# Performance work log

Measured on AMD Instinct MI355X. Metric: run time of the kernel, lower is better.

Reference implementation:

```python
import jax, jax.numpy as jnp
import numpy as np

B, S, DM = 2, 2048, 1024
H, DH = 16, 64
SCALE = jnp.sqrt(jnp.float32(DH))  # dot_scale = sqrt(dim_head)


def setup_inputs() -> dict:
    key = jax.random.key(0)
    ks = jax.random.split(key, 9)
    std = 1.0 / np.sqrt(DM)
    x = jax.random.normal(ks[0], (B, S, DM), dtype=jnp.float32)
    Wq = jax.random.uniform(ks[1], (DM, DM), jnp.float32, -std, std)
    bq = jax.random.uniform(ks[2], (DM,), jnp.float32, -std, std)
    Wk = jax.random.uniform(ks[3], (DM, DM), jnp.float32, -std, std)
    bk = jax.random.uniform(ks[4], (DM,), jnp.float32, -std, std)
    Wv = jax.random.uniform(ks[5], (DM, DM), jnp.float32, -std, std)
    bv = jax.random.uniform(ks[6], (DM,), jnp.float32, -std, std)
    Wo = jax.random.uniform(ks[7], (DM, DM), jnp.float32, -std, std)
    bo = jax.random.uniform(ks[8], (DM,), jnp.float32, -std, std)
    # causal mask: 1 = masked (future positions), broadcast over batch
    causal = jnp.triu(jnp.ones((S, S), dtype=jnp.int32), k=1)
    attention_mask = jnp.broadcast_to(causal, (B, S, S))
    return {"x": x, "Wq": Wq, "bq": bq, "Wk": Wk, "bk": bk,
            "Wv": Wv, "bv": bv, "Wo": Wo, "bo": bo,
            "attention_mask": attention_mask}


def reference(x, Wq, bq, Wk, bk, Wv, bv, Wo, bo, attention_mask):
    # Linear layers (torch nn.Linear: y = x @ W^T + b)
    q = (x @ Wq.T + bq).reshape(B, S, H, DH).transpose(0, 2, 1, 3)  # (B,H,S,DH)
    k = (x @ Wk.T + bk).reshape(B, S, H, DH).transpose(0, 2, 1, 3)  # (B,H,S,DH)
    v = (x @ Wv.T + bv).reshape(B, S, H, DH).transpose(0, 2, 1, 3)  # (B,H,S,DH)
    # scores: (B,H,S,S), then mask==1 -> -inf, softmax over last dim
    scores = jnp.einsum('bhsd,bhtd->bhst', q, k) / SCALE
    mask = attention_mask[:, None, :, :]  # (B,1,S,S)
    scores = jnp.where(mask == 1, -jnp.inf, scores)
    attn = jax.nn.softmax(scores, axis=-1)
    # dropout is identity in eval mode
    ctx = jnp.einsum('bhst,bhtd->bshd', attn, v).reshape(B, S, H * DH)
    return ctx @ Wo.T + bo
```

## Files before the change

kernel.cpp:

```cpp
#include <hip/hip_runtime.h>
#include <stdint.h>

typedef unsigned short u16;
typedef __attribute__((ext_vector_type(8))) short bf16x8;
typedef __attribute__((ext_vector_type(4))) float f32x4;

#define BATCH 2
#define S_LEN 2048
#define DMODEL 1024
#define NH 16
#define DHEAD 64
#define MTOT 4096
#define QSCALE 0.18033688011112042f

#define GL2LDS(g, l) \
  __builtin_amdgcn_global_load_lds((const __attribute__((address_space(1))) void*)(g), \
                                   (__attribute__((address_space(3))) void*)(l), 16, 0, 0)

__device__ __forceinline__ u16 f2bf(float x) {
  union { float f; uint32_t u; } v; v.f = x;
  uint32_t r = v.u + 0x7fffu + ((v.u >> 16) & 1u);
  return (u16)(r >> 16);
}
__device__ __forceinline__ u16 f2bf_fast(float x) {
  union { float f; uint32_t u; } v; v.f = x;
  return (u16)((v.u + 0x8000u) >> 16);
}

struct CvtArgs {
  const float* src[5];
  u16* dst[5];
};

__global__ __launch_bounds__(256) void cvt_all(CvtArgs a) {
  int bx = blockIdx.x;
  int region, off;
  if (bx < 4096) { region = 0; off = bx; }
  else { region = 1 + ((bx - 4096) >> 10); off = (bx - 4096) & 1023; }
  const float* s = a.src[region];
  u16* d = a.dst[region];
  int i = (off * 256 + threadIdx.x) * 4;
  float4 v = *(const float4*)(s + i);
  uint2 pk;
  pk.x = (uint32_t)f2bf(v.x) | ((uint32_t)f2bf(v.y) << 16);
  pk.y = (uint32_t)f2bf(v.z) | ((uint32_t)f2bf(v.w) << 16);
  *(uint2*)(d + i) = pk;
}

__device__ __forceinline__ void gemm_body(const u16* __restrict__ A,
                                          const u16* __restrict__ W,
                                          const float* __restrict__ bias,
                                          void* __restrict__ out,
                                          int mode, float scale) {
  __shared__ u16 As[128 * 32];
  __shared__ u16 Bs[128 * 32];
  const int tid = threadIdx.x;
  const int m0 = blockIdx.y * 128;
  const int n0 = blockIdx.x * 128;
  const int wave = tid >> 6, lane = tid & 63;
  const int wm = (wave >> 1) * 64, wn = (wave & 1) * 64;
  const int quad = lane >> 4, l15 = lane & 15;

  const int row0 = tid >> 2, g0 = ((tid & 3) ^ (row0 & 3)) * 8;
  const int row1 = (tid + 256) >> 2, g1 = ((tid & 3) ^ (row1 & 3)) * 8;
  const int lb0 = wave * 512;
  const int lb1 = 2048 + wave * 512;
  const int xk = (quad ^ (l15 & 3)) * 8;

  f32x4 acc[4][4] = {};

  for (int kt = 0; kt < DMODEL; kt += 32) {
    GL2LDS(A + (size_t)(m0 + row0) * DMODEL + kt + g0, As + lb0);
    GL2LDS(A + (size_t)(m0 + row1) * DMODEL + kt + g1, As + lb1);
    GL2LDS(W + (size_t)(n0 + row0) * DMODEL + kt + g0, Bs + lb0);
    GL2LDS(W + (size_t)(n0 + row1) * DMODEL + kt + g1, Bs + lb1);
    __syncthreads();
    bf16x8 af[4], bfr[4];
#pragma unroll
    for (int bi = 0; bi < 4; ++bi)
      af[bi] = *(const bf16x8*)(&As[(wm + bi * 16 + l15) * 32 + xk]);
#pragma unroll
    for (int bj = 0; bj < 4; ++bj)
      bfr[bj] = *(const bf16x8*)(&Bs[(wn + bj * 16 + l15) * 32 + xk]);
#pragma unroll
    for (int bi = 0; bi < 4; ++bi)
#pragma unroll
      for (int bj = 0; bj < 4; ++bj)
        acc[bi][bj] = __builtin_amdgcn_mfma_f32_16x16x32_bf16(af[bi], bfr[bj], acc[bi][bj], 0, 0, 0);
    __syncthreads();
  }

#pragma unroll
  for (int bi = 0; bi < 4; ++bi) {
#pragma unroll
    for (int bj = 0; bj < 4; ++bj) {
      int n = n0 + wn + bj * 16 + l15;
      float bval = bias[n];
#pragma unroll
      for (int r = 0; r < 4; ++r) {
        int m = m0 + wm + bi * 16 + quad * 4 + r;
        float v = (acc[bi][bj][r] + bval) * scale;
        u16 bvu = f2bf(v);
        int b = m >> 11, s = m & 2047;
        int h = n >> 6, d = n & 63;
        size_t bh = (size_t)(b * NH + h);
        if (mode == 1)
          ((u16*)out)[(bh * S_LEN + s) * DHEAD + d] = bvu;
        else
          ((u16*)out)[((bh * 256 + (s >> 3)) * 64 + d) * 8 + (s & 7)] = bvu;
      }
    }
  }
}

struct QKVArgs {
  const u16* w[3];
  const float* b[3];
  u16* o[3];
};

__global__ __launch_bounds__(256) void qkv_gemm(const u16* __restrict__ xb, QKVArgs a) {
  int z = blockIdx.z;
  int mode = (z == 2) ? 2 : 1;
  float scale = (z == 0) ? QSCALE : 1.0f;
  gemm_body(xb, a.w[z], a.b[z], a.o[z], mode, scale);
}

__global__ __launch_bounds__(256) void out_gemm(const u16* __restrict__ A,
                                                const u16* __restrict__ W,
                                                const float* __restrict__ bias,
                                                float* __restrict__ out) {
  __shared__ u16 As[128 * 32];
  __shared__ u16 Bs[64 * 32];
  const int tid = threadIdx.x;
  const int m0 = blockIdx.y * 128;
  const int n0 = blockIdx.x * 64;
  const int wave = tid >> 6, lane = tid & 63;
  const int wm = (wave >> 1) * 64, wn = (wave & 1) * 32;
  const int quad = lane >> 4, l15 = lane & 15;

  const int row0 = tid >> 2, g0 = ((tid & 3) ^ (row0 & 3)) * 8;
  const int row1 = (tid + 256) >> 2, g1 = ((tid & 3) ^ (row1 & 3)) * 8;
  const int lb0 = wave * 512;
  const int lb1 = 2048 + wave * 512;
  const int xk = (quad ^ (l15 & 3)) * 8;

  f32x4 acc[4][2] = {};

  for (int kt = 0; kt < DMODEL; kt += 32) {
    GL2LDS(A + (size_t)(m0 + row0) * DMODEL + kt + g0, As + lb0);
    GL2LDS(A + (size_t)(m0 + row1) * DMODEL + kt + g1, As + lb1);
    GL2LDS(W + (size_t)(n0 + row0) * DMODEL + kt + g0, Bs + lb0);
    __syncthreads();
    bf16x8 af[4], bfr[2];
#pragma unroll
    for (int bi = 0; bi < 4; ++bi)
      af[bi] = *(const bf16x8*)(&As[(wm + bi * 16 + l15) * 32 + xk]);
#pragma unroll
    for (int bj = 0; bj < 2; ++bj)
      bfr[bj] = *(const bf16x8*)(&Bs[(wn + bj * 16 + l15) * 32 + xk]);
#pragma unroll
    for (int bi = 0; bi < 4; ++bi)
#pragma unroll
      for (int bj = 0; bj < 2; ++bj)
        acc[bi][bj] = __builtin_amdgcn_mfma_f32_16x16x32_bf16(af[bi], bfr[bj], acc[bi][bj], 0, 0, 0);
    __syncthreads();
  }

#pragma unroll
  for (int bi = 0; bi < 4; ++bi) {
#pragma unroll
    for (int bj = 0; bj < 2; ++bj) {
      int n = n0 + wn + bj * 16 + l15;
      float bval = bias[n];
#pragma unroll
      for (int r = 0; r < 4; ++r) {
        int m = m0 + wm + bi * 16 + quad * 4 + r;
        out[(size_t)m * DMODEL + n] = acc[bi][bj][r] + bval;
      }
    }
  }
}

__global__ __launch_bounds__(256) void attn(const u16* __restrict__ Q,
                                            const u16* __restrict__ Kg,
                                            const u16* __restrict__ Vt8,
                                            u16* __restrict__ ctx) {
  __shared__ u16 Kd[2][128 * 64];
  __shared__ u16 Vd[2][64 * 128];
  __shared__ u16 Ps[64 * 80];
  const int tid = threadIdx.x;
  const int qp = blockIdx.x >> 5;
  const int bh = blockIdx.x & 31;
  const int wave = tid >> 6, lane = tid & 63;
  const int quad = lane >> 4, l15 = lane & 15;
  const size_t base = (size_t)bh * S_LEN * DHEAD;
  const int b = bh >> 4, h = bh & 15;
  const int xk7 = l15 & 7;

#define STAGE(kt_, pb)                                                                   \
  do {                                                                                   \
    _Pragma("unroll")                                                                    \
    for (int i_ = 0; i_ < 4; ++i_) {                                                     \
      int c_ = tid + 256 * i_;                                                           \
      int row_ = c_ >> 3, g_ = ((c_ & 7) ^ (row_ & 7)) * 8;                              \
      GL2LDS(Kg + base + (size_t)((kt_) * 128 + row_) * 64 + g_,                         \
             &Kd[pb][0] + i_ * 2048 + wave * 512);                                       \
      GL2LDS(Vt8 + base + (size_t)((kt_) * 1024 + c_) * 8,                               \
             &Vd[pb][0] + i_ * 2048 + wave * 512);                                       \
    }                                                                                    \
  } while (0)

  for (int half = 0; half < 2; ++half) {
    const int qt = half ? (31 - qp) : qp;
    const int qrow = qt * 64 + wave * 16 + l15;
    bf16x8 qf0 = *(const bf16x8*)(Q + base + (size_t)qrow * DHEAD + quad * 8);
    bf16x8 qf1 = *(const bf16x8*)(Q + base + (size_t)qrow * DHEAD + 32 + quad * 8);

    float l_part[4] = {0.f, 0.f, 0.f, 0.f};
    f32x4 o[4] = {};

    const int ktmax = qt >> 1;
    STAGE(0, 0);

    for (int kt = 0; kt <= ktmax; ++kt) {
      const int p = kt & 1;
      __syncthreads();
      if (kt < ktmax) STAGE(kt + 1, p ^ 1);

      const bool diag = (kt == ktmax);
      const int qg_max = qt * 64 + wave * 16 + 15;
      f32x4 s_acc[8];
#pragma unroll
      for (int bj = 0; bj < 8; ++bj) {
        if (diag && (kt * 128 + bj * 16 > qg_max)) {
          s_acc[bj] = f32x4{-1e30f, -1e30f, -1e30f, -1e30f};
          continue;
        }
        const int krow = (bj * 16 + l15) * 64;
        bf16x8 kf0 = *(const bf16x8*)(&Kd[p][krow + ((quad ^ xk7) * 8)]);
        bf16x8 kf1 = *(const bf16x8*)(&Kd[p][krow + (((quad + 4) ^ xk7) * 8)]);
        f32x4 t = {0.f, 0.f, 0.f, 0.f};
        t = __builtin_amdgcn_mfma_f32_16x16x32_bf16(qf0, kf0, t, 0, 0, 0);
        t = __builtin_amdgcn_mfma_f32_16x16x32_bf16(qf1, kf1, t, 0, 0, 0);
        s_acc[bj] = t;
      }

      if (diag) {
#pragma unroll
        for (int bj = 0; bj < 8; ++bj) {
          int kg = kt * 128 + bj * 16 + l15;
#pragma unroll
          for (int r = 0; r < 4; ++r) {
            int qg = qt * 64 + wave * 16 + quad * 4 + r;
            if (kg > qg) s_acc[bj][r] = -1e30f;
          }
        }
      }

#pragma unroll
      for (int ph = 0; ph < 2; ++ph) {
        if (diag && (kt * 128 + ph * 64 > qg_max)) continue;
#pragma unroll
        for (int bj2 = 0; bj2 < 4; ++bj2) {
          int bj = ph * 4 + bj2;
#pragma unroll
          for (int r = 0; r < 4; ++r) {
            float pv = exp2f(s_acc[bj][r]);
            l_part[r] += pv;
            Ps[(wave * 16 + quad * 4 + r) * 80 + bj2 * 16 + l15] = f2bf_fast(pv);
          }
        }
#pragma unroll
        for (int kk2 = 0; kk2 < 2; ++kk2) {
          bf16x8 pf = *(const bf16x8*)(&Ps[(wave * 16 + l15) * 80 + kk2 * 32 + quad * 8]);
          int kk = ph * 2 + kk2;
#pragma unroll
          for (int dj = 0; dj < 4; ++dj) {
            bf16x8 vf = *(const bf16x8*)(&Vd[p][((kk * 4 + quad) * 64 + dj * 16 + l15) * 8]);
            o[dj] = __builtin_amdgcn_mfma_f32_16x16x32_bf16(pf, vf, o[dj], 0, 0, 0);
          }
        }
      }
    }

    __syncthreads();

#pragma unroll
    for (int r = 0; r < 4; ++r) {
      float s = l_part[r];
      s += __shfl_xor(s, 1, 64);
      s += __shfl_xor(s, 2, 64);
      s += __shfl_xor(s, 4, 64);
      s += __shfl_xor(s, 8, 64);
      float inv = 1.0f / s;
      int srow = qt * 64 + wave * 16 + quad * 4 + r;
      size_t rowbase = ((size_t)b * S_LEN + srow) * DMODEL + h * DHEAD;
#pragma unroll
      for (int dj = 0; dj < 4; ++dj)
        ctx[rowbase + dj * 16 + l15] = f2bf(o[dj][r] * inv);
    }
  }
#undef STAGE
}

extern "C" void kernel_launch(void* const* d_in, const int* in_sizes, int n_in,
                              void* d_out, int out_size, void* d_ws, size_t ws_size,
                              hipStream_t stream) {
  const float* x  = (const float*)d_in[0];
  const float* Wq = (const float*)d_in[1];
  const float* bq = (const float*)d_in[2];
  const float* Wk = (const float*)d_in[3];
  const float* bk = (const float*)d_in[4];
  const float* Wv = (const float*)d_in[5];
  const float* bv = (const float*)d_in[6];
  const float* Wo = (const float*)d_in[7];
  const float* bo = (const float*)d_in[8];
  float* out = (float*)d_out;

  char* ws = (char*)d_ws;
  const size_t MB = 1u << 20;
  u16* xb   = (u16*)(ws + 0);
  u16* ctxb = xb;
  u16* wqb  = (u16*)(ws + 8 * MB);
  u16* wkb  = (u16*)(ws + 10 * MB);
  u16* wvb  = (u16*)(ws + 12 * MB);
  u16* wob  = (u16*)(ws + 14 * MB);
  u16* qb   = (u16*)(ws + 16 * MB);
  u16* kb   = (u16*)(ws + 24 * MB);
  u16* vtb  = (u16*)(ws + 32 * MB);

  CvtArgs c;
  c.src[0] = x;  c.dst[0] = xb;
  c.src[1] = Wq; c.dst[1] = wqb;
  c.src[2] = Wk; c.dst[2] = wkb;
  c.src[3] = Wv; c.dst[3] = wvb;
  c.src[4] = Wo; c.dst[4] = wob;
  cvt_all<<<4096 + 4 * 1024, 256, 0, stream>>>(c);

  QKVArgs a;
  a.w[0] = wqb; a.w[1] = wkb; a.w[2] = wvb;
  a.b[0] = bq;  a.b[1] = bk;  a.b[2] = bv;
  a.o[0] = qb;  a.o[1] = kb;  a.o[2] = vtb;
  qkv_gemm<<<dim3(DMODEL / 128, MTOT / 128, 3), 256, 0, stream>>>(xb, a);

  attn<<<512, 256, 0, stream>>>(qb, kb, vtb, ctxb);

  out_gemm<<<dim3(DMODEL / 64, MTOT / 128), 256, 0, stream>>>(ctxb, wob, bo, out);
}
```

Baseline: 208.6 us.

## Shrink attention KV tile to 64 and launch one block per query tile

The attention kernel now uses 64-row K/V tiles instead of 128 and launches 1024 blocks, each owning a single query tile, instead of 512 blocks that each processed a pair of tiles. Query tiles are assigned to blocks with a zig-zag ordering to balance causal work across the grid, and the P scratch buffer gets an XOR swizzle in place of padding. Shared memory per block drops, and launch_bounds now requests 4 blocks per CU, which should raise occupancy and trim wasted work on the diagonal tile. In exchange there are more loop iterations and barriers per unit of work, and register pressure is capped by the occupancy hint.

After: 210.0 us. No clear change (+0.7%).

```diff
diff --git a/kernel.cpp b/kernel.cpp
--- a/kernel.cpp
+++ b/kernel.cpp
@@ -182,16 +182,19 @@
   }
 }
 
-__global__ __launch_bounds__(256) void attn(const u16* __restrict__ Q,
-                                            const u16* __restrict__ Kg,
-                                            const u16* __restrict__ Vt8,
-                                            u16* __restrict__ ctx) {
-  __shared__ u16 Kd[2][128 * 64];
-  __shared__ u16 Vd[2][64 * 128];
-  __shared__ u16 Ps[64 * 80];
+__global__ __launch_bounds__(256, 4) void attn(const u16* __restrict__ Q,
+                                               const u16* __restrict__ Kg,
+                                               const u16* __restrict__ Vt8,
+                                               u16* __restrict__ ctx) {
+  __shared__ u16 Kd[2][64 * 64];
+  __shared__ u16 Vd[2][64 * 64];
+  __shared__ u16 Ps[64 * 64];
   const int tid = threadIdx.x;
-  const int qp = blockIdx.x >> 5;
+  const int g = blockIdx.x >> 5;
   const int bh = blockIdx.x & 31;
+  const int gv = g & 7;
+  int qt = (g & 8) ? (15 - gv) : gv;
+  if (g & 16) qt += 16;
   const int wave = tid >> 6, lane = tid & 63;
   const int quad = lane >> 4, l15 = lane & 15;
   const size_t base = (size_t)bh * S_LEN * DHEAD;
@@ -201,105 +204,98 @@
 #define STAGE(kt_, pb)                                                                   \
   do {                                                                                   \
     _Pragma("unroll")                                                                    \
-    for (int i_ = 0; i_ < 4; ++i_) {                                                     \
+    for (int i_ = 0; i_ < 2; ++i_) {                                                     \
       int c_ = tid + 256 * i_;                                                           \
       int row_ = c_ >> 3, g_ = ((c_ & 7) ^ (row_ & 7)) * 8;                              \
-      GL2LDS(Kg + base + (size_t)((kt_) * 128 + row_) * 64 + g_,                         \
+      GL2LDS(Kg + base + (size_t)((kt_) * 64 + row_) * 64 + g_,                          \
              &Kd[pb][0] + i_ * 2048 + wave * 512);                                       \
-      GL2LDS(Vt8 + base + (size_t)((kt_) * 1024 + c_) * 8,                               \
+      GL2LDS(Vt8 + base + (size_t)((kt_) * 512 + c_) * 8,                                \
              &Vd[pb][0] + i_ * 2048 + wave * 512);                                       \
     }                                                                                    \
   } while (0)
 
-  for (int half = 0; half < 2; ++half) {
-    const int qt = half ? (31 - qp) : qp;
-    const int qrow = qt * 64 + wave * 16 + l15;
-    bf16x8 qf0 = *(const bf16x8*)(Q + base + (size_t)qrow * DHEAD + quad * 8);
-    bf16x8 qf1 = *(const bf16x8*)(Q + base + (size_t)qrow * DHEAD + 32 + quad * 8);
-
-    float l_part[4] = {0.f, 0.f, 0.f, 0.f};
-    f32x4 o[4] = {};
-
-    const int ktmax = qt >> 1;
-    STAGE(0, 0);
-
-    for (int kt = 0; kt <= ktmax; ++kt) {
-      const int p = kt & 1;
-      __syncthreads();
-      if (kt < ktmax) STAGE(kt + 1, p ^ 1);
-
-      const bool diag = (kt == ktmax);
-      const int qg_max = qt * 64 + wave * 16 + 15;
-      f32x4 s_acc[8];
-#pragma unroll
-      for (int bj = 0; bj < 8; ++bj) {
-        if (diag && (kt * 128 + bj * 16 > qg_max)) {
-          s_acc[bj] = f32x4{-1e30f, -1e30f, -1e30f, -1e30f};
-          continue;
+  const int qrow = qt * 64 + wave * 16 + l15;
+  bf16x8 qf0 = *(const bf16x8*)(Q + base + (size_t)qrow * DHEAD + quad * 8);
+  bf16x8 qf1 = *(const bf16x8*)(Q + base + (size_t)qrow * DHEAD + 32 + quad * 8);
+
+  float l_part[4] = {0.f, 0.f, 0.f, 0.f};
+  f32x4 o[4] = {};
+
+  STAGE(0, 0);
+
+  for (int kt = 0; kt <= qt; ++kt) {
+    const int p = kt & 1;
+    __syncthreads();
+    if (kt < qt) STAGE(kt + 1, p ^ 1);
+
+    const bool diag = (kt == qt);
+    f32x4 s_acc[4];
+#pragma unroll
+    for (int bj = 0; bj < 4; ++bj) {
+      if (diag && bj > wave) {
+        s_acc[bj] = f32x4{-1e30f, -1e30f, -1e30f, -1e30f};
+        continue;
+      }
+      const int krow = (bj * 16 + l15) * 64;
+      bf16x8 kf0 = *(const bf16x8*)(&Kd[p][krow + ((quad ^ xk7) * 8)]);
+      bf16x8 kf1 = *(const bf16x8*)(&Kd[p][krow + (((quad + 4) ^ xk7) * 8)]);
+      f32x4 t = {0.f, 0.f, 0.f, 0.f};
+      t = __builtin_amdgcn_mfma_f32_16x16x32_bf16(qf0, kf0, t, 0, 0, 0);
+      t = __builtin_amdgcn_mfma_f32_16x16x32_bf16(qf1, kf1, t, 0, 0, 0);
+      s_acc[bj] = t;
+    }
+
+    if (diag) {
+#pragma unroll
+      for (int bj = 0; bj < 4; ++bj) {
+        int kg = kt * 64 + bj * 16 + l15;
+#pragma unroll
+        for (int r = 0; r < 4; ++r) {
+          int qg = qt * 64 + wave * 16 + quad * 4 + r;
+          if (kg > qg) s_acc[bj][r] = -1e30f;
         }
-        const int krow = (bj * 16 + l15) * 64;
-        bf16x8 kf0 = *(const bf16x8*)(&Kd[p][krow + ((quad ^ xk7) * 8)]);
-        bf16x8 kf1 = *(const bf16x8*)(&Kd[p][krow + (((quad + 4) ^ xk7) * 8)]);
-        f32x4 t = {0.f, 0.f, 0.f, 0.f};
-        t = __builtin_amdgcn_mfma_f32_16x16x32_bf16(qf0, kf0, t, 0, 0, 0);
-        t = __builtin_amdgcn_mfma_f32_16x16x32_bf16(qf1, kf1, t, 0, 0, 0);
-        s_acc[bj] = t;
-      }
-
-      if (diag) {
-#pragma unroll
-        for (int bj = 0; bj < 8; ++bj) {
-          int kg = kt * 128 + bj * 16 + l15;
-#pragma unroll
-          for (int r = 0; r < 4; ++r) {
-            int qg = qt * 64 + wave * 16 + quad * 4 + r;
-            if (kg > qg) s_acc[bj][r] = -1e30f;
-          }
+      }
+    }
+
+#pragma unroll
+    for (int bj = 0; bj < 4; ++bj) {
+#pragma unroll
+      for (int r = 0; r < 4; ++r) {
+        float pv = exp2f(s_acc[bj][r]);
+        l_part[r] += pv;
+        int row = wave * 16 + quad * 4 + r;
+        int ch = (bj * 2 + (l15 >> 3)) ^ (row & 7);
+        Ps[row * 64 + ch * 8 + (l15 & 7)] = f2bf_fast(pv);
+      }
+    }
+
+    {
+      const int row2 = wave * 16 + l15;
+#pragma unroll
+      for (int kk = 0; kk < 2; ++kk) {
+        bf16x8 pf = *(const bf16x8*)(&Ps[row2 * 64 + (((kk << 2) + quad) ^ xk7) * 8]);
+#pragma unroll
+        for (int dj = 0; dj < 4; ++dj) {
+          bf16x8 vf = *(const bf16x8*)(&Vd[p][((kk * 4 + quad) * 64 + dj * 16 + l15) * 8]);
+          o[dj] = __builtin_amdgcn_mfma_f32_16x16x32_bf16(pf, vf, o[dj], 0, 0, 0);
         }
       }
-
-#pragma unroll
-      for (int ph = 0; ph < 2; ++ph) {
-        if (diag && (kt * 128 + ph * 64 > qg_max)) continue;
-#pragma unroll
-        for (int bj2 = 0; bj2 < 4; ++bj2) {
-          int bj = ph * 4 + bj2;
-#pragma unroll
-          for (int r = 0; r < 4; ++r) {
-            float pv = exp2f(s_acc[bj][r]);
-            l_part[r] += pv;
-            Ps[(wave * 16 + quad * 4 + r) * 80 + bj2 * 16 + l15] = f2bf_fast(pv);
-          }
-        }
-#pragma unroll
-        for (int kk2 = 0; kk2 < 2; ++kk2) {
-          bf16x8 pf = *(const bf16x8*)(&Ps[(wave * 16 + l15) * 80 + kk2 * 32 + quad * 8]);
-          int kk = ph * 2 + kk2;
-#pragma unroll
-          for (int dj = 0; dj < 4; ++dj) {
-            bf16x8 vf = *(const bf16x8*)(&Vd[p][((kk * 4 + quad) * 64 + dj * 16 + l15) * 8]);
-            o[dj] = __builtin_amdgcn_mfma_f32_16x16x32_bf16(pf, vf, o[dj], 0, 0, 0);
-          }
-        }
-      }
-    }
-
-    __syncthreads();
-
-#pragma unroll
-    for (int r = 0; r < 4; ++r) {
-      float s = l_part[r];
-      s += __shfl_xor(s, 1, 64);
-      s += __shfl_xor(s, 2, 64);
-      s += __shfl_xor(s, 4, 64);
-      s += __shfl_xor(s, 8, 64);
-      float inv = 1.0f / s;
-      int srow = qt * 64 + wave * 16 + quad * 4 + r;
-      size_t rowbase = ((size_t)b * S_LEN + srow) * DMODEL + h * DHEAD;
-#pragma unroll
-      for (int dj = 0; dj < 4; ++dj)
-        ctx[rowbase + dj * 16 + l15] = f2bf(o[dj][r] * inv);
-    }
+    }
+  }
+
+#pragma unroll
+  for (int r = 0; r < 4; ++r) {
+    float s = l_part[r];
+    s += __shfl_xor(s, 1, 64);
+    s += __shfl_xor(s, 2, 64);
+    s += __shfl_xor(s, 4, 64);
+    s += __shfl_xor(s, 8, 64);
+    float inv = 1.0f / s;
+    int srow = qt * 64 + wave * 16 + quad * 4 + r;
+    size_t rowbase = ((size_t)b * S_LEN + srow) * DMODEL + h * DHEAD;
+#pragma unroll
+    for (int dj = 0; dj < 4; ++dj)
+      ctx[rowbase + dj * 16 + l15] = f2bf(o[dj][r] * inv);
   }
 #undef STAGE
 }
@@ -344,7 +340,7 @@
   a.o[0] = qb;  a.o[1] = kb;  a.o[2] = vtb;
   qkv_gemm<<<dim3(DMODEL / 128, MTOT / 128, 3), 256, 0, stream>>>(xb, a);
 
-  attn<<<512, 256, 0, stream>>>(qb, kb, vtb, ctxb);
+  attn<<<1024, 256, 0, stream>>>(qb, kb, vtb, ctxb);
 
   out_gemm<<<dim3(DMODEL / 64, MTOT / 128), 256, 0, stream>>>(ctxb, wob, bo, out);
 }
```
